# Kernel optimization log

Measured on AMD Instinct MI355X. Metric: run time of the kernel, lower is better.

Reference implementation:

```python
import jax, jax.numpy as jnp
import numpy as np
from jax import lax

K_EDGE = 4096  # fixed padded size for per-(b,c) edge point sets


def _min_pool2d_3x3(x):
    # torch: -max_pool2d(-x, 3, 1, 1); maxpool pads with -inf, so minpool pads with +inf
    return lax.reduce_window(x, jnp.inf, lax.min,
                             (1, 1, 3, 3), (1, 1, 1, 1),
                             [(0, 0), (0, 0), (1, 1), (1, 1)])


def _get_edges(mask):
    ero = _min_pool2d_3x3(mask)
    return jnp.logical_xor(ero > 0.5, mask > 0.5)  # [B,C,H,W] bool


def _ahd_loss_one(gedge, pedge, coords):
    # gedge, pedge: [N] bool flattened edge masks; coords: [N,2] float32 pixel coords
    n_g = gedge.sum().astype(jnp.float32)
    n_p = pedge.sum().astype(jnp.float32)
    ar = jnp.arange(K_EDGE)
    gidx = jnp.nonzero(gedge, size=K_EDGE, fill_value=0)[0]
    pidx = jnp.nonzero(pedge, size=K_EDGE, fill_value=0)[0]
    gvalid = ar < n_g
    pvalid = ar < n_p
    gc = coords[gidx]  # [K,2]
    pc = coords[pidx]  # [K,2]
    # pairwise Euclidean distances [K,K]
    d = jnp.sqrt(((gc[:, None, :] - pc[None, :, :]) ** 2).sum(-1))
    # for each gth edge point: distance to nearest pred edge point (== EDT of pred edges)
    dg = jnp.min(jnp.where(pvalid[None, :], d, jnp.inf), axis=1)
    gth2pred = jnp.where(gvalid, dg, 0.0).sum() / n_g
    # for each pred edge point: distance to nearest gth edge point
    dp = jnp.min(jnp.where(gvalid[:, None], d, jnp.inf), axis=0)
    pred2gth = jnp.where(pvalid, dp, 0.0).sum() / n_p
    ahd = (gth2pred + pred2gth) / 2.0
    ahd = jnp.where((n_g == 0) & (n_p == 0), jnp.nan, ahd)
    return 1.0 - 1.0 / (1.0 + ahd)


def setup_inputs() -> dict:
    key = jax.random.key(0)
    B, C, H, W = 8, 2, 256, 256
    k1, k2 = jax.random.split(key)
    # smooth blob-like soft masks: low-res noise upsampled -> realistic contours
    gth = jax.image.resize(jax.random.uniform(k1, (B, C, 12, 12), jnp.float32),
                           (B, C, H, W), method='bilinear')
    pred = jax.image.resize(jax.random.uniform(k2, (B, C, 12, 12), jnp.float32),
                            (B, C, H, W), method='bilinear')
    return {"gth": gth, "pred": pred}


def reference(gth, pred):
    B, C, H, W = gth.shape
    gth_b = (gth > 0.5).astype(jnp.float32)
    pred_b = (pred > 0.5).astype(jnp.float32)
    gedges = _get_edges(gth_b).reshape(B * C, H * W)
    pedges = _get_edges(pred_b).reshape(B * C, H * W)
    yy, xx = jnp.meshgrid(jnp.arange(H), jnp.arange(W), indexing='ij')
    coords = jnp.stack([yy, xx], axis=-1).reshape(H * W, 2).astype(jnp.float32)
    losses = jax.vmap(_ahd_loss_one, in_axes=(0, 0, None))(gedges, pedges, coords)
    return jnp.nanmean(losses)
```

## Files before the change

### kernel.cpp

```cpp
#include <hip/hip_runtime.h>
#include <math.h>

#define HH 256
#define WW 256
#define HWSZ (HH * WW)
#define KE 4096
#define NSLICE 16
#define NCH 64
#define GSENT 1024
#define RPB 32

typedef unsigned long long u64;
typedef unsigned short u16;

__global__ void __launch_bounds__(256) binarize_pack(
        const float* __restrict__ gth, const float* __restrict__ pred,
        u64* __restrict__ bm) {
    int b = blockIdx.x;
    int tensor = b >> 12;
    int sr = b & 4095;
    const float* img = tensor ? pred : gth;
    float v = img[sr * WW + threadIdx.x];
    u64 bal = __ballot(v > 0.5f);
    int lane = threadIdx.x & 63;
    int wave = threadIdx.x >> 6;
    if (lane == 0) bm[(size_t)b * 4 + wave] = bal;
}

__global__ void __launch_bounds__(256) edge_compact(
        const u64* __restrict__ bm,
        float2* __restrict__ gpts, float2* __restrict__ ppts,
        u64* __restrict__ ebm,
        int* __restrict__ gcnt, int* __restrict__ pcnt) {
    int b = blockIdx.x;
    int tensor = b >> 4;
    int slice = b & 15;
    const u64* rm = bm + (size_t)(tensor * 4096 + slice * 256) * 4;
    float2* pts = (tensor ? ppts : gpts) + slice * KE;
    int* cnt = (tensor ? pcnt : gcnt) + slice;
    u64* eb = ebm + (size_t)b * 1024;

    int row = threadIdx.x;
    u64 vc[4], va[4], vb[4];
#pragma unroll
    for (int w = 0; w < 4; ++w) {
        vc[w] = rm[row * 4 + w];
        va[w] = (row > 0) ? rm[(row - 1) * 4 + w] : ~0ull;
        vb[w] = (row < HH - 1) ? rm[(row + 1) * 4 + w] : ~0ull;
    }
    u64 vert[4];
#pragma unroll
    for (int w = 0; w < 4; ++w) vert[w] = va[w] & vc[w] & vb[w];
    u64 e[4];
#pragma unroll
    for (int w = 0; w < 4; ++w) {
        u64 left  = (vert[w] << 1) | ((w > 0) ? (vert[w - 1] >> 63) : 1ull);
        u64 right = (vert[w] >> 1) | (((w < 3) ? (vert[w + 1] & 1ull) : 1ull) << 63);
        e[w] = vc[w] & ~(vert[w] & left & right);
    }
    int mycnt = __popcll(e[0]) + __popcll(e[1]) + __popcll(e[2]) + __popcll(e[3]);

    __shared__ int sc[256];
    sc[row] = mycnt;
    __syncthreads();
    for (int d = 1; d < 256; d <<= 1) {
        int v = (row >= d) ? sc[row - d] : 0;
        __syncthreads();
        sc[row] += v;
        __syncthreads();
    }
    int off = sc[row] - mycnt;

    int rem = KE - off;
    u64 t[4];
    if (rem >= mycnt) {
#pragma unroll
        for (int w = 0; w < 4; ++w) t[w] = e[w];
    } else if (rem <= 0) {
#pragma unroll
        for (int w = 0; w < 4; ++w) t[w] = 0ull;
    } else {
        int k = rem;
#pragma unroll
        for (int w = 0; w < 4; ++w) {
            int pc = __popcll(e[w]);
            if (k >= pc) { t[w] = e[w]; k -= pc; }
            else {
                u64 bits = e[w], keep = 0ull;
                for (int i = 0; i < k; ++i) {
                    u64 low = bits & (~bits + 1ull);
                    keep |= low;
                    bits ^= low;
                }
                t[w] = keep;
                k = 0;
            }
        }
    }
#pragma unroll
    for (int w = 0; w < 4; ++w) eb[row * 4 + w] = t[w];

    int o = off;
#pragma unroll
    for (int w = 0; w < 4; ++w) {
        u64 bits = e[w];
        while (bits) {
            int l = __ffsll((long long)bits) - 1;
            bits &= bits - 1;
            if (o < KE) pts[o] = make_float2((float)row, (float)(w * 64 + l));
            ++o;
        }
    }
    if (row == HH - 1) *cnt = sc[HH - 1];
}

__device__ __forceinline__ int word_dist(u64 w, int p) {
    if (w == 0) return GSENT;
    int lo = __ffsll((long long)w) - 1;
    int hi = 63 - __clzll((long long)w);
    if (p <= lo) return lo - p;
    if (p >= hi) return p - hi;
    u64 up = w >> p;
    int du = __ffsll((long long)up) - 1;
    u64 dn = w << (63 - p);
    int dd = __clzll((long long)dn);
    return min(du, dd);
}

__global__ void __launch_bounds__(256) edt_vert(
        const u64* __restrict__ ebm, u16* __restrict__ G16) {
    int map = blockIdx.x >> 3;
    int rblk = blockIdx.x & 7;
    const u64* eb = ebm + (size_t)map * 1024;
    u16* G = G16 + (size_t)map * HWSZ;

    __shared__ u64 ebl[1024];
    int tid = threadIdx.x;
    for (int i = tid; i < 1024; i += 256) ebl[i] = eb[i];
    __syncthreads();

    int c = tid, cw = c >> 6, cb = c & 63;
    u64 w0 = 0, w1 = 0, w2 = 0, w3 = 0;
#pragma unroll 4
    for (int r = 0; r < 64; ++r) {
        w0 |= ((ebl[(r      ) * 4 + cw] >> cb) & 1ull) << r;
        w1 |= ((ebl[(r +  64) * 4 + cw] >> cb) & 1ull) << r;
        w2 |= ((ebl[(r + 128) * 4 + cw] >> cb) & 1ull) << r;
        w3 |= ((ebl[(r + 192) * 4 + cw] >> cb) & 1ull) << r;
    }

    int r0 = rblk * RPB;
#pragma unroll 4
    for (int i = 0; i < RPB; ++i) {
        int r = r0 + i;
        int d = word_dist(w0, r);
        d = min(d, word_dist(w1, r - 64));
        d = min(d, word_dist(w2, r - 128));
        d = min(d, word_dist(w3, r - 192));
        G[r * WW + c] = (u16)min(d, GSENT);
    }
}

__global__ void __launch_bounds__(64) nn_gather(
        const float2* __restrict__ gpts, const float2* __restrict__ ppts,
        const int* __restrict__ gcnt, const int* __restrict__ pcnt,
        const u16* __restrict__ G16, float* __restrict__ partial) {
    int b = blockIdx.x;
    int chunk = b & (NCH - 1);
    int sd = b >> 6;
    int dir = sd & 1;
    int slice = sd >> 1;
    int tid = threadIdx.x;

    int qfull = dir ? pcnt[slice] : gcnt[slice];
    int qc = min(qfull, KE);
    int qi = chunk * 64 + tid;

    float val = 0.0f;
    if (qi < qc) {
        const float2* q = (dir ? ppts : gpts) + slice * KE;
        int tt = dir ? 0 : 1;
        const u16* G = G16 + (size_t)(tt * 16 + slice) * HWSZ;
        float2 qp = q[qi];
        int r = (int)qp.x, c = (int)qp.y;
        const int4* grow = (const int4*)(G + r * WW);
        int m = 0x7fffffff;
#pragma unroll
        for (int j = 0; j < 32; ++j) {
            int4 v = grow[j];
            int base = j * 8;
#define STEP(word, k0)                                                      \
            {                                                               \
                int g0 = (word) & 0xffff;                                   \
                int g1 = (int)(((unsigned)(word)) >> 16);                   \
                int dc0 = c - (base + k0);                                  \
                int dc1 = c - (base + k0 + 1);                              \
                m = min(m, dc0 * dc0 + g0 * g0);                            \
                m = min(m, dc1 * dc1 + g1 * g1);                            \
            }
            STEP(v.x, 0) STEP(v.y, 2) STEP(v.z, 4) STEP(v.w, 6)
#undef STEP
        }
        val = sqrtf((float)m);
    }
    for (int s = 32; s > 0; s >>= 1) val += __shfl_xor(val, s, 64);
    if (tid == 0) partial[b] = val;
}

__global__ void __launch_bounds__(512) finalize3(
        const int* __restrict__ gcnt, const int* __restrict__ pcnt,
        const float* __restrict__ partial, float* __restrict__ out) {
    int tid = threadIdx.x;
    float v = partial[tid * 4] + partial[tid * 4 + 1] +
              partial[tid * 4 + 2] + partial[tid * 4 + 3];
    v += __shfl_xor(v, 1, 16);
    v += __shfl_xor(v, 2, 16);
    v += __shfl_xor(v, 4, 16);
    v += __shfl_xor(v, 8, 16);
    __shared__ float sdsum[32];
    if ((tid & 15) == 0) sdsum[tid >> 4] = v;
    __syncthreads();
    if (tid == 0) {
        float sum = 0.0f;
        int nvalid = 0;
        for (int s = 0; s < NSLICE; ++s) {
            int ng = gcnt[s];
            int np_ = pcnt[s];
            if (ng > 0 && np_ > 0) {
                float ahd = 0.5f * (sdsum[s * 2 + 0] / (float)ng +
                                    sdsum[s * 2 + 1] / (float)np_);
                sum += 1.0f - 1.0f / (1.0f + ahd);
                nvalid++;
            }
        }
        out[0] = nvalid ? (sum / (float)nvalid) : NAN;
    }
}

extern "C" void kernel_launch(void* const* d_in, const int* in_sizes, int n_in,
                              void* d_out, int out_size, void* d_ws, size_t ws_size,
                              hipStream_t stream) {
    const float* gth = (const float*)d_in[0];
    const float* pred = (const float*)d_in[1];
    float* out = (float*)d_out;
    char* ws = (char*)d_ws;

    u64* bm = (u64*)(ws);
    u64* ebm = (u64*)(ws + 262144);
    float2* gpts = (float2*)(ws + 524288);
    float2* ppts = (float2*)(ws + 1048576);
    u16* G16 = (u16*)(ws + 1572864);
    int* gcnt = (int*)(ws + 5767168);
    int* pcnt = (int*)(ws + 5767232);
    float* partial = (float*)(ws + 5767296);

    binarize_pack<<<8192, 256, 0, stream>>>(gth, pred, bm);
    edge_compact<<<32, 256, 0, stream>>>(bm, gpts, ppts, ebm, gcnt, pcnt);
    edt_vert<<<256, 256, 0, stream>>>(ebm, G16);
    nn_gather<<<NSLICE * 2 * NCH, 64, 0, stream>>>(gpts, ppts, gcnt, pcnt, G16, partial);
    finalize3<<<1, 512, 0, stream>>>(gcnt, pcnt, partial, out);
}
```

Baseline: 46.74 us.

## Fuse binarize into edge compaction and finalize into gather via last-block atomic

```diff
diff --git a/kernel.cpp b/kernel.cpp
--- a/kernel.cpp
+++ b/kernel.cpp
@@ -7,111 +7,123 @@
 #define KE 4096
 #define NSLICE 16
 #define NCH 64
+#define NBLK_NN (NSLICE * 2 * NCH)
 #define GSENT 1024
 #define RPB 32
 
 typedef unsigned long long u64;
 typedef unsigned short u16;
 
-__global__ void __launch_bounds__(256) binarize_pack(
+__global__ void __launch_bounds__(1024) edge_fused(
         const float* __restrict__ gth, const float* __restrict__ pred,
-        u64* __restrict__ bm) {
-    int b = blockIdx.x;
-    int tensor = b >> 12;
-    int sr = b & 4095;
-    const float* img = tensor ? pred : gth;
-    float v = img[sr * WW + threadIdx.x];
-    u64 bal = __ballot(v > 0.5f);
-    int lane = threadIdx.x & 63;
-    int wave = threadIdx.x >> 6;
-    if (lane == 0) bm[(size_t)b * 4 + wave] = bal;
-}
-
-__global__ void __launch_bounds__(256) edge_compact(
-        const u64* __restrict__ bm,
         float2* __restrict__ gpts, float2* __restrict__ ppts,
         u64* __restrict__ ebm,
-        int* __restrict__ gcnt, int* __restrict__ pcnt) {
+        int* __restrict__ gcnt, int* __restrict__ pcnt,
+        int* __restrict__ counter) {
     int b = blockIdx.x;
     int tensor = b >> 4;
     int slice = b & 15;
-    const u64* rm = bm + (size_t)(tensor * 4096 + slice * 256) * 4;
+    const float* img = (tensor ? pred : gth) + slice * HWSZ;
     float2* pts = (tensor ? ppts : gpts) + slice * KE;
     int* cnt = (tensor ? pcnt : gcnt) + slice;
     u64* eb = ebm + (size_t)b * 1024;
 
-    int row = threadIdx.x;
-    u64 vc[4], va[4], vb[4];
-#pragma unroll
-    for (int w = 0; w < 4; ++w) {
-        vc[w] = rm[row * 4 + w];
-        va[w] = (row > 0) ? rm[(row - 1) * 4 + w] : ~0ull;
-        vb[w] = (row < HH - 1) ? rm[(row + 1) * 4 + w] : ~0ull;
-    }
-    u64 vert[4];
-#pragma unroll
-    for (int w = 0; w < 4; ++w) vert[w] = va[w] & vc[w] & vb[w];
+    int tid = threadIdx.x;
+    if (b == 0 && tid == 0) *counter = 0;
+
+    __shared__ u64 bm_l[1024];
+    __shared__ int wsum[4];
+
+    int prow = tid >> 8;
+    int pcol = tid & 255;
+    int wword = (tid >> 6) & 3;
+    int plane = tid & 63;
+#pragma unroll 8
+    for (int i = 0; i < 64; ++i) {
+        int r = i * 4 + prow;
+        float v = img[r * WW + pcol];
+        u64 bal = __ballot(v > 0.5f);
+        if (plane == 0) bm_l[r * 4 + wword] = bal;
+    }
+    __syncthreads();
+
     u64 e[4];
-#pragma unroll
-    for (int w = 0; w < 4; ++w) {
-        u64 left  = (vert[w] << 1) | ((w > 0) ? (vert[w - 1] >> 63) : 1ull);
-        u64 right = (vert[w] >> 1) | (((w < 3) ? (vert[w + 1] & 1ull) : 1ull) << 63);
-        e[w] = vc[w] & ~(vert[w] & left & right);
-    }
-    int mycnt = __popcll(e[0]) + __popcll(e[1]) + __popcll(e[2]) + __popcll(e[3]);
-
-    __shared__ int sc[256];
-    sc[row] = mycnt;
-    __syncthreads();
-    for (int d = 1; d < 256; d <<= 1) {
-        int v = (row >= d) ? sc[row - d] : 0;
-        __syncthreads();
-        sc[row] += v;
-        __syncthreads();
-    }
-    int off = sc[row] - mycnt;
-
-    int rem = KE - off;
-    u64 t[4];
-    if (rem >= mycnt) {
-#pragma unroll
-        for (int w = 0; w < 4; ++w) t[w] = e[w];
-    } else if (rem <= 0) {
-#pragma unroll
-        for (int w = 0; w < 4; ++w) t[w] = 0ull;
-    } else {
-        int k = rem;
+    int mycnt = 0, incl = 0, off = 0;
+    int row = tid, lane = tid & 63, wv = tid >> 6;
+    if (tid < 256) {
+        u64 vc[4], va[4], vb[4];
 #pragma unroll
         for (int w = 0; w < 4; ++w) {
-            int pc = __popcll(e[w]);
-            if (k >= pc) { t[w] = e[w]; k -= pc; }
-            else {
-                u64 bits = e[w], keep = 0ull;
-                for (int i = 0; i < k; ++i) {
-                    u64 low = bits & (~bits + 1ull);
-                    keep |= low;
-                    bits ^= low;
+            vc[w] = bm_l[row * 4 + w];
+            va[w] = (row > 0) ? bm_l[(row - 1) * 4 + w] : ~0ull;
+            vb[w] = (row < HH - 1) ? bm_l[(row + 1) * 4 + w] : ~0ull;
+        }
+        u64 vert[4];
+#pragma unroll
+        for (int w = 0; w < 4; ++w) vert[w] = va[w] & vc[w] & vb[w];
+#pragma unroll
+        for (int w = 0; w < 4; ++w) {
+            u64 left  = (vert[w] << 1) | ((w > 0) ? (vert[w - 1] >> 63) : 1ull);
+            u64 right = (vert[w] >> 1) | (((w < 3) ? (vert[w + 1] & 1ull) : 1ull) << 63);
+            e[w] = vc[w] & ~(vert[w] & left & right);
+        }
+        mycnt = __popcll(e[0]) + __popcll(e[1]) + __popcll(e[2]) + __popcll(e[3]);
+
+        incl = mycnt;
+        for (int d = 1; d < 64; d <<= 1) {
+            int n = __shfl_up(incl, d, 64);
+            if (lane >= d) incl += n;
+        }
+        if (lane == 63) wsum[wv] = incl;
+    }
+    __syncthreads();
+    if (tid < 256) {
+        int wpre = 0;
+        for (int k = 0; k < 4; ++k) wpre += (k < wv) ? wsum[k] : 0;
+        off = wpre + incl - mycnt;
+
+        int rem = KE - off;
+        u64 t[4];
+        if (rem >= mycnt) {
+#pragma unroll
+            for (int w = 0; w < 4; ++w) t[w] = e[w];
+        } else if (rem <= 0) {
+#pragma unroll
+            for (int w = 0; w < 4; ++w) t[w] = 0ull;
+        } else {
+            int k = rem;
+#pragma unroll
+            for (int w = 0; w < 4; ++w) {
+                int pc = __popcll(e[w]);
+                if (k >= pc) { t[w] = e[w]; k -= pc; }
+                else {
+                    u64 bits = e[w], keep = 0ull;
+                    for (int i = 0; i < k; ++i) {
+                        u64 low = bits & (~bits + 1ull);
+                        keep |= low;
+                        bits ^= low;
+                    }
+                    t[w] = keep;
+                    k = 0;
                 }
-                t[w] = keep;
-                k = 0;
-            }
-        }
-    }
-#pragma unroll
-    for (int w = 0; w < 4; ++w) eb[row * 4 + w] = t[w];
-
-    int o = off;
-#pragma unroll
-    for (int w = 0; w < 4; ++w) {
-        u64 bits = e[w];
-        while (bits) {
-            int l = __ffsll((long long)bits) - 1;
-            bits &= bits - 1;
-            if (o < KE) pts[o] = make_float2((float)row, (float)(w * 64 + l));
-            ++o;
-        }
-    }
-    if (row == HH - 1) *cnt = sc[HH - 1];
+            }
+        }
+#pragma unroll
+        for (int w = 0; w < 4; ++w) eb[row * 4 + w] = t[w];
+
+        int o = off;
+#pragma unroll
+        for (int w = 0; w < 4; ++w) {
+            u64 bits = e[w];
+            while (bits) {
+                int l = __ffsll((long long)bits) - 1;
+                bits &= bits - 1;
+                if (o < KE) pts[o] = make_float2((float)row, (float)(w * 64 + l));
+                ++o;
+            }
+        }
+        if (row == HH - 1) *cnt = wpre + incl;
+    }
 }
 
 __device__ __forceinline__ int word_dist(u64 w, int p) {
@@ -164,7 +176,8 @@
 __global__ void __launch_bounds__(64) nn_gather(
         const float2* __restrict__ gpts, const float2* __restrict__ ppts,
         const int* __restrict__ gcnt, const int* __restrict__ pcnt,
-        const u16* __restrict__ G16, float* __restrict__ partial) {
+        const u16* __restrict__ G16, float* __restrict__ partial,
+        int* __restrict__ counter, float* __restrict__ out) {
     int b = blockIdx.x;
     int chunk = b & (NCH - 1);
     int sd = b >> 6;
@@ -204,36 +217,42 @@
         val = sqrtf((float)m);
     }
     for (int s = 32; s > 0; s >>= 1) val += __shfl_xor(val, s, 64);
-    if (tid == 0) partial[b] = val;
-}
-
-__global__ void __launch_bounds__(512) finalize3(
-        const int* __restrict__ gcnt, const int* __restrict__ pcnt,
-        const float* __restrict__ partial, float* __restrict__ out) {
-    int tid = threadIdx.x;
-    float v = partial[tid * 4] + partial[tid * 4 + 1] +
-              partial[tid * 4 + 2] + partial[tid * 4 + 3];
-    v += __shfl_xor(v, 1, 16);
-    v += __shfl_xor(v, 2, 16);
-    v += __shfl_xor(v, 4, 16);
-    v += __shfl_xor(v, 8, 16);
-    __shared__ float sdsum[32];
-    if ((tid & 15) == 0) sdsum[tid >> 4] = v;
-    __syncthreads();
+
+    __shared__ int s_last;
     if (tid == 0) {
-        float sum = 0.0f;
-        int nvalid = 0;
-        for (int s = 0; s < NSLICE; ++s) {
-            int ng = gcnt[s];
-            int np_ = pcnt[s];
-            if (ng > 0 && np_ > 0) {
-                float ahd = 0.5f * (sdsum[s * 2 + 0] / (float)ng +
-                                    sdsum[s * 2 + 1] / (float)np_);
-                sum += 1.0f - 1.0f / (1.0f + ahd);
-                nvalid++;
-            }
-        }
-        out[0] = nvalid ? (sum / (float)nvalid) : NAN;
+        __hip_atomic_store(&partial[b], val, __ATOMIC_RELEASE,
+                           __HIP_MEMORY_SCOPE_AGENT);
+        int prev = __hip_atomic_fetch_add(counter, 1, __ATOMIC_ACQ_REL,
+                                          __HIP_MEMORY_SCOPE_AGENT);
+        s_last = (prev == NBLK_NN - 1) ? 1 : 0;
+    }
+    __syncthreads();
+    if (s_last) {
+        __shared__ float sdsum[32];
+        if (tid < 32) {
+            float s = 0.0f;
+            for (int k = 0; k < NCH; ++k)
+                s += __hip_atomic_load(&partial[tid * NCH + k],
+                                       __ATOMIC_RELAXED,
+                                       __HIP_MEMORY_SCOPE_AGENT);
+            sdsum[tid] = s;
+        }
+        __syncthreads();
+        if (tid == 0) {
+            float sum = 0.0f;
+            int nvalid = 0;
+            for (int s = 0; s < NSLICE; ++s) {
+                int ng = gcnt[s];
+                int np_ = pcnt[s];
+                if (ng > 0 && np_ > 0) {
+                    float ahd = 0.5f * (sdsum[s * 2 + 0] / (float)ng +
+                                        sdsum[s * 2 + 1] / (float)np_);
+                    sum += 1.0f - 1.0f / (1.0f + ahd);
+                    nvalid++;
+                }
+            }
+            out[0] = nvalid ? (sum / (float)nvalid) : NAN;
+        }
     }
 }
 
@@ -245,18 +264,18 @@
     float* out = (float*)d_out;
     char* ws = (char*)d_ws;
 
-    u64* bm = (u64*)(ws);
-    u64* ebm = (u64*)(ws + 262144);
-    float2* gpts = (float2*)(ws + 524288);
-    float2* ppts = (float2*)(ws + 1048576);
-    u16* G16 = (u16*)(ws + 1572864);
-    int* gcnt = (int*)(ws + 5767168);
-    int* pcnt = (int*)(ws + 5767232);
-    float* partial = (float*)(ws + 5767296);
-
-    binarize_pack<<<8192, 256, 0, stream>>>(gth, pred, bm);
-    edge_compact<<<32, 256, 0, stream>>>(bm, gpts, ppts, ebm, gcnt, pcnt);
+    u64* ebm = (u64*)(ws);
+    float2* gpts = (float2*)(ws + 262144);
+    float2* ppts = (float2*)(ws + 786432);
+    u16* G16 = (u16*)(ws + 1310720);
+    int* gcnt = (int*)(ws + 5505024);
+    int* pcnt = (int*)(ws + 5505088);
+    float* partial = (float*)(ws + 5505152);
+    int* counter = (int*)(ws + 5513344);
+
+    edge_fused<<<32, 1024, 0, stream>>>(gth, pred, gpts, ppts, ebm,
+                                        gcnt, pcnt, counter);
     edt_vert<<<256, 256, 0, stream>>>(ebm, G16);
-    nn_gather<<<NSLICE * 2 * NCH, 64, 0, stream>>>(gpts, ppts, gcnt, pcnt, G16, partial);
-    finalize3<<<1, 512, 0, stream>>>(gcnt, pcnt, partial, out);
-}
+    nn_gather<<<NBLK_NN, 64, 0, stream>>>(gpts, ppts, gcnt, pcnt, G16,
+                                          partial, counter, out);
+}
```

After: 105.4 us. 2.25x slower.

## Fuse vertical EDT into nearest-neighbor gather using per-block shared-memory distance map

Applied to the files above, without the earlier changes.

```diff
diff --git a/kernel.cpp b/kernel.cpp
--- a/kernel.cpp
+++ b/kernel.cpp
@@ -6,9 +6,8 @@
 #define HWSZ (HH * WW)
 #define KE 4096
 #define NSLICE 16
-#define NCH 64
+#define NCHD 8
 #define GSENT 1024
-#define RPB 32
 
 typedef unsigned long long u64;
 typedef unsigned short u16;
@@ -22,9 +21,7 @@
     const float* img = tensor ? pred : gth;
     float v = img[sr * WW + threadIdx.x];
     u64 bal = __ballot(v > 0.5f);
-    int lane = threadIdx.x & 63;
-    int wave = threadIdx.x >> 6;
-    if (lane == 0) bm[(size_t)b * 4 + wave] = bal;
+    if ((threadIdx.x & 63) == 0) bm[(size_t)b * 4 + (threadIdx.x >> 6)] = bal;
 }
 
 __global__ void __launch_bounds__(256) edge_compact(
@@ -114,28 +111,29 @@
     if (row == HH - 1) *cnt = sc[HH - 1];
 }
 
-__device__ __forceinline__ int word_dist(u64 w, int p) {
-    if (w == 0) return GSENT;
-    int lo = __ffsll((long long)w) - 1;
-    int hi = 63 - __clzll((long long)w);
-    if (p <= lo) return lo - p;
-    if (p >= hi) return p - hi;
-    u64 up = w >> p;
-    int du = __ffsll((long long)up) - 1;
-    u64 dn = w << (63 - p);
-    int dd = __clzll((long long)dn);
-    return min(du, dd);
-}
-
-__global__ void __launch_bounds__(256) edt_vert(
-        const u64* __restrict__ ebm, u16* __restrict__ G16) {
-    int map = blockIdx.x >> 3;
-    int rblk = blockIdx.x & 7;
-    const u64* eb = ebm + (size_t)map * 1024;
-    u16* G = G16 + (size_t)map * HWSZ;
-
-    __shared__ u64 ebl[1024];
+__device__ __forceinline__ int gidx(int r, int c) {
+    int cj = (c >> 3) ^ (r & 7);
+    return r * WW + cj * 8 + (c & 7);
+}
+
+__global__ void __launch_bounds__(256) edt_nn(
+        const float2* __restrict__ gpts, const float2* __restrict__ ppts,
+        const int* __restrict__ gcnt, const int* __restrict__ pcnt,
+        const u64* __restrict__ ebm, float* __restrict__ partial) {
+    extern __shared__ char smem[];
+    u64* ebl = (u64*)smem;
+    u16* G   = (u16*)(smem + 8192);
+    __shared__ float red[4];
+
+    int b = blockIdx.x;
+    int chunk = b & (NCHD - 1);
+    int sd = b >> 3;
+    int dir = sd & 1;
+    int slice = sd >> 1;
     int tid = threadIdx.x;
+
+    int tt = dir ? 0 : 1;
+    const u64* eb = ebm + (size_t)(tt * 16 + slice) * 1024;
     for (int i = tid; i < 1024; i += 256) ebl[i] = eb[i];
     __syncthreads();
 
@@ -148,77 +146,75 @@
         w2 |= ((ebl[(r + 128) * 4 + cw] >> cb) & 1ull) << r;
         w3 |= ((ebl[(r + 192) * 4 + cw] >> cb) & 1ull) << r;
     }
-
-    int r0 = rblk * RPB;
-#pragma unroll 4
-    for (int i = 0; i < RPB; ++i) {
-        int r = r0 + i;
-        int d = word_dist(w0, r);
-        d = min(d, word_dist(w1, r - 64));
-        d = min(d, word_dist(w2, r - 128));
-        d = min(d, word_dist(w3, r - 192));
-        G[r * WW + c] = (u16)min(d, GSENT);
-    }
-}
-
-__global__ void __launch_bounds__(64) nn_gather(
-        const float2* __restrict__ gpts, const float2* __restrict__ ppts,
-        const int* __restrict__ gcnt, const int* __restrict__ pcnt,
-        const u16* __restrict__ G16, float* __restrict__ partial) {
-    int b = blockIdx.x;
-    int chunk = b & (NCH - 1);
-    int sd = b >> 6;
-    int dir = sd & 1;
-    int slice = sd >> 1;
-    int tid = threadIdx.x;
+    int g = GSENT;
+#define DPASS(wrd, base)                                                    \
+    for (int i = 0; i < 64; ++i) {                                          \
+        int bit = (int)((wrd >> i) & 1ull);                                 \
+        g = bit ? 0 : min(g + 1, GSENT);                                    \
+        G[gidx(base + i, c)] = (u16)g;                                      \
+    }
+    DPASS(w0, 0) DPASS(w1, 64) DPASS(w2, 128) DPASS(w3, 192)
+#undef DPASS
+    g = GSENT;
+#define UPASS(wrd, base)                                                    \
+    for (int i = 63; i >= 0; --i) {                                         \
+        int bit = (int)((wrd >> i) & 1ull);                                 \
+        g = bit ? 0 : min(g + 1, GSENT);                                    \
+        int ix = gidx(base + i, c);                                         \
+        G[ix] = (u16)min((int)G[ix], g);                                    \
+    }
+    UPASS(w3, 192) UPASS(w2, 128) UPASS(w1, 64) UPASS(w0, 0)
+#undef UPASS
+    __syncthreads();
 
     int qfull = dir ? pcnt[slice] : gcnt[slice];
     int qc = min(qfull, KE);
-    int qi = chunk * 64 + tid;
-
+    const float2* q = (dir ? ppts : gpts) + slice * KE;
     float val = 0.0f;
-    if (qi < qc) {
-        const float2* q = (dir ? ppts : gpts) + slice * KE;
-        int tt = dir ? 0 : 1;
-        const u16* G = G16 + (size_t)(tt * 16 + slice) * HWSZ;
-        float2 qp = q[qi];
-        int r = (int)qp.x, c = (int)qp.y;
-        const int4* grow = (const int4*)(G + r * WW);
-        int m = 0x7fffffff;
-#pragma unroll
-        for (int j = 0; j < 32; ++j) {
-            int4 v = grow[j];
-            int base = j * 8;
+#pragma unroll
+    for (int k = 0; k < 2; ++k) {
+        int qi = chunk * 512 + k * 256 + tid;
+        if (qi < qc) {
+            float2 qp = q[qi];
+            int r = (int)qp.x, cc = (int)qp.y;
+            const uint4* grow = (const uint4*)(G + r * WW);
+            int rsw = r & 7;
+            int m = 0x7fffffff;
+#pragma unroll
+            for (int j = 0; j < 32; ++j) {
+                uint4 v = grow[j ^ rsw];
+                int bs = j * 8;
 #define STEP(word, k0)                                                      \
-            {                                                               \
-                int g0 = (word) & 0xffff;                                   \
-                int g1 = (int)(((unsigned)(word)) >> 16);                   \
-                int dc0 = c - (base + k0);                                  \
-                int dc1 = c - (base + k0 + 1);                              \
-                m = min(m, dc0 * dc0 + g0 * g0);                            \
-                m = min(m, dc1 * dc1 + g1 * g1);                            \
+                {                                                           \
+                    int g0 = (int)((word) & 0xffffu);                       \
+                    int g1 = (int)((word) >> 16);                           \
+                    int d0 = cc - (bs + k0);                                \
+                    int d1 = cc - (bs + k0 + 1);                            \
+                    m = min(m, d0 * d0 + g0 * g0);                          \
+                    m = min(m, d1 * d1 + g1 * g1);                          \
+                }
+                STEP(v.x, 0) STEP(v.y, 2) STEP(v.z, 4) STEP(v.w, 6)
+#undef STEP
             }
-            STEP(v.x, 0) STEP(v.y, 2) STEP(v.z, 4) STEP(v.w, 6)
-#undef STEP
-        }
-        val = sqrtf((float)m);
+            val += sqrtf((float)m);
+        }
     }
     for (int s = 32; s > 0; s >>= 1) val += __shfl_xor(val, s, 64);
-    if (tid == 0) partial[b] = val;
-}
-
-__global__ void __launch_bounds__(512) finalize3(
+    if ((tid & 63) == 0) red[tid >> 6] = val;
+    __syncthreads();
+    if (tid == 0) partial[b] = red[0] + red[1] + red[2] + red[3];
+}
+
+__global__ void __launch_bounds__(256) finalize4(
         const int* __restrict__ gcnt, const int* __restrict__ pcnt,
         const float* __restrict__ partial, float* __restrict__ out) {
     int tid = threadIdx.x;
-    float v = partial[tid * 4] + partial[tid * 4 + 1] +
-              partial[tid * 4 + 2] + partial[tid * 4 + 3];
-    v += __shfl_xor(v, 1, 16);
-    v += __shfl_xor(v, 2, 16);
-    v += __shfl_xor(v, 4, 16);
-    v += __shfl_xor(v, 8, 16);
     __shared__ float sdsum[32];
-    if ((tid & 15) == 0) sdsum[tid >> 4] = v;
+    if (tid < 32) {
+        float s = 0.0f;
+        for (int k = 0; k < NCHD; ++k) s += partial[tid * NCHD + k];
+        sdsum[tid] = s;
+    }
     __syncthreads();
     if (tid == 0) {
         float sum = 0.0f;
@@ -249,14 +245,13 @@
     u64* ebm = (u64*)(ws + 262144);
     float2* gpts = (float2*)(ws + 524288);
     float2* ppts = (float2*)(ws + 1048576);
-    u16* G16 = (u16*)(ws + 1572864);
-    int* gcnt = (int*)(ws + 5767168);
-    int* pcnt = (int*)(ws + 5767232);
-    float* partial = (float*)(ws + 5767296);
+    int* gcnt = (int*)(ws + 1572864);
+    int* pcnt = (int*)(ws + 1572928);
+    float* partial = (float*)(ws + 1572992);
 
     binarize_pack<<<8192, 256, 0, stream>>>(gth, pred, bm);
     edge_compact<<<32, 256, 0, stream>>>(bm, gpts, ppts, ebm, gcnt, pcnt);
-    edt_vert<<<256, 256, 0, stream>>>(ebm, G16);
-    nn_gather<<<NSLICE * 2 * NCH, 64, 0, stream>>>(gpts, ppts, gcnt, pcnt, G16, partial);
-    finalize3<<<1, 512, 0, stream>>>(gcnt, pcnt, partial, out);
-}
+    edt_nn<<<32 * NCHD, 256, 139264, stream>>>(gpts, ppts, gcnt, pcnt,
+                                               ebm, partial);
+    finalize4<<<1, 256, 0, stream>>>(gcnt, pcnt, partial, out);
+}
```

Result: slower. 53.55 us (+14.6%).
